# Kernel optimization log

Hardware: AMD Instinct MI355X
Metric: run time of the kernel (lower is better)

Reference implementation:

```python
import jax, jax.numpy as jnp
import numpy as np

HEADS = 16
DIM_HEAD = 64
QUERY_DIM = 1024
CONTEXT_DIM = 1024
INNER = HEADS * DIM_HEAD  # 1024


def setup_inputs() -> dict:
    key = jax.random.key(0)
    k1, k2, k3, k4, k5, k6, k7 = jax.random.split(key, 7)
    b, nq, nk = 2, 2048, 2048
    q = jax.random.normal(k1, (b, nq, QUERY_DIM), dtype=jnp.float32)
    context = jax.random.normal(k2, (b, nk, CONTEXT_DIM), dtype=jnp.float32)
    # True = masked out (filled with -inf); keep sparse so no row is fully masked
    mask = jax.random.randint(k3, (b, nk), 0, 2).astype(bool) & jax.random.randint(k7, (b, nk), 0, 2).astype(bool)
    s = 0.02
    Wq = jax.random.normal(k4, (QUERY_DIM, INNER), dtype=jnp.float32) * s
    Wkv = jax.random.normal(k5, (CONTEXT_DIM, 2 * INNER), dtype=jnp.float32) * s
    Wout = jax.random.normal(k6, (INNER, QUERY_DIM), dtype=jnp.float32) * s
    b_out = jnp.zeros((QUERY_DIM,), dtype=jnp.float32)
    return {"q": q, "context": context, "mask": mask, "Wq": Wq, "Wkv": Wkv, "Wout": Wout, "b_out": b_out}


def reference(q, context, mask, Wq, Wkv, Wout, b_out):
    b, nq, _ = q.shape
    nk = context.shape[1]
    h, dh = HEADS, DIM_HEAD
    scale = dh ** -0.5
    qp = q @ Wq                              # [b, nq, h*dh]
    k, v = jnp.split(context @ Wkv, 2, -1)   # each [b, nk, h*dh]
    qh = qp.reshape(b, nq, h, dh).transpose(0, 2, 1, 3)  # [b, h, nq, dh]
    kh = k.reshape(b, nk, h, dh).transpose(0, 2, 1, 3)
    vh = v.reshape(b, nk, h, dh).transpose(0, 2, 1, 3)
    attn = jnp.einsum('bhid,bhjd->bhij', qh, kh) * scale  # [b, h, nq, nk]
    attn = jnp.where(mask[:, None, None, :], -jnp.inf, attn)
    attn = jax.nn.softmax(attn, axis=-1)
    out = jnp.einsum('bhij,bhjd->bhid', attn, vh)         # [b, h, nq, dh]
    out = out.transpose(0, 2, 1, 3).reshape(b, nq, h * dh)
    return out @ Wout + b_out
```

## Files before the change

kernel.cpp:

```cpp
#include <hip/hip_runtime.h>
#include <stdint.h>

typedef unsigned short u16;
typedef __attribute__((ext_vector_type(8))) short bf16x8;
typedef __attribute__((ext_vector_type(4))) float f32x4;
typedef __attribute__((ext_vector_type(4))) u16 u16x4;

#define DEVI __device__ __forceinline__

DEVI u16 f2bf(float x){
  uint32_t u = __float_as_uint(x);
  u += 0x7fffu + ((u >> 16) & 1u);
  return (u16)(u >> 16);
}

DEVI void gload_lds16(const void* g, void* l){
  __builtin_amdgcn_global_load_lds((__attribute__((address_space(1))) const void*)g,
                                   (__attribute__((address_space(3))) void*)l,
                                   16, 0, 0);
}

__global__ __launch_bounds__(256) void k_prep(const float* __restrict__ q,
                                              const float* __restrict__ ctx,
                                              const int* __restrict__ m,
                                              u16* __restrict__ qb, u16* __restrict__ cb,
                                              float* __restrict__ mf){
  const int b = blockIdx.x;
  if (b < 2048){
    const float* s = (b < 1024) ? q : ctx;
    u16* d = (b < 1024) ? qb : cb;
    const int base = (b & 1023) << 12;
    #pragma unroll
    for (int it = 0; it < 4; ++it){
      const int i = base + (it << 10) + (threadIdx.x << 2);
      const float4 v = *(const float4*)(s + i);
      u16x4 o = { f2bf(v.x), f2bf(v.y), f2bf(v.z), f2bf(v.w) };
      *(u16x4*)(d + i) = o;
    }
  } else {
    for (int i = threadIdx.x; i < 4096; i += 256) mf[i] = m[i] ? -1e30f : 0.0f;
  }
}

__global__ __launch_bounds__(256) void k_tr3(const float* __restrict__ Wq,
                                             const float* __restrict__ Wkv,
                                             const float* __restrict__ Wo,
                                             u16* __restrict__ WqT, u16* __restrict__ WkvT,
                                             u16* __restrict__ WoT){
  const int z = blockIdx.z;
  if (z != 1 && blockIdx.x >= 16) return;
  const float* s = (z == 0) ? Wq : (z == 1) ? Wkv : Wo;
  u16* d = (z == 0) ? WqT : (z == 1) ? WkvT : WoT;
  const int R = 1024, C = (z == 1) ? 2048 : 1024;
  __shared__ float t[64][65];
  const int x = threadIdx.x, y = threadIdx.y;
  const int r0 = blockIdx.y * 64, c0 = blockIdx.x * 64;
  #pragma unroll
  for (int yy = y; yy < 64; yy += 4) t[yy][x] = s[(size_t)(r0 + yy) * C + c0 + x];
  __syncthreads();
  #pragma unroll
  for (int yy = y; yy < 64; yy += 4) d[(size_t)(c0 + yy) * R + r0 + x] = f2bf(t[x][yy]);
}

__global__ __launch_bounds__(256, 2)
void k_gemm01(const u16* __restrict__ Aq, const u16* __restrict__ Ac,
              const u16* __restrict__ Bq, const u16* __restrict__ Bkv,
              u16* __restrict__ QPb, u16* __restrict__ Kbb, u16* __restrict__ Vtb)
{
  __shared__ __align__(16) u16 As[128 * 64];
  __shared__ __align__(16) u16 Bs[128 * 64];
  const int tid = threadIdx.x;
  const int lane = tid & 63, wave = tid >> 6;
  const int g = lane >> 4, l16 = lane & 15;
  const int bx = blockIdx.x;
  const bool isq = bx < 8;
  const u16* A = isq ? Aq : Ac;
  const u16* B = isq ? Bq : Bkv;
  const int brow = blockIdx.y << 7, bcol = (isq ? bx : bx - 8) << 7;
  const int wr = wave >> 1, wc = wave & 1;
  f32x4 acc[4][4] = {};

  for (int kt = 0; kt < 16; ++kt){
    const int k0 = kt << 6;
    #pragma unroll
    for (int i = 0; i < 4; ++i){
      const int c = i * 256 + tid;
      const int row = c >> 3;
      const int sc = ((c & 7) ^ (row & 7)) << 3;
      gload_lds16(A + (size_t)(brow + row) * 1024 + k0 + sc, (char*)As + (i * 4 + wave) * 1024);
      gload_lds16(B + (size_t)(bcol + row) * 1024 + k0 + sc, (char*)Bs + (i * 4 + wave) * 1024);
    }
    __syncthreads();
    #pragma unroll
    for (int kk = 0; kk < 2; ++kk){
      bf16x8 a[4], b[4];
      #pragma unroll
      for (int mi = 0; mi < 4; ++mi){
        const int r = wr * 64 + mi * 16 + l16;
        a[mi] = *(const bf16x8*)((const char*)As + r * 128 + (((kk << 6) + (g << 4)) ^ ((r & 7) << 4)));
      }
      #pragma unroll
      for (int ni = 0; ni < 4; ++ni){
        const int r = wc * 64 + ni * 16 + l16;
        b[ni] = *(const bf16x8*)((const char*)Bs + r * 128 + (((kk << 6) + (g << 4)) ^ ((r & 7) << 4)));
      }
      #pragma unroll
      for (int mi = 0; mi < 4; ++mi)
        #pragma unroll
        for (int ni = 0; ni < 4; ++ni)
          acc[mi][ni] = __builtin_amdgcn_mfma_f32_16x16x32_bf16(a[mi], b[ni], acc[mi][ni], 0, 0, 0);
    }
    __syncthreads();
  }

  #pragma unroll
  for (int mi = 0; mi < 4; ++mi){
    #pragma unroll
    for (int ni = 0; ni < 4; ++ni){
      #pragma unroll
      for (int r = 0; r < 4; ++r){
        const int row = brow + wr * 64 + mi * 16 + g * 4 + r;
        const int col = bcol + wc * 64 + ni * 16 + l16;
        const float v = acc[mi][ni][r];
        const int bb = row >> 11, qi = row & 2047;
        if (isq){
          const int h = col >> 6, dd = col & 63;
          QPb[(size_t)((bb << 4) + h) * 131072 + (qi << 6) + dd] = f2bf(v * 0.125f);
        } else if (col < 1024){
          const int h = col >> 6, dd = col & 63;
          Kbb[(size_t)((bb << 4) + h) * 131072 + (qi << 6) + dd] = f2bf(v);
        } else {
          const int c2 = col - 1024, h = c2 >> 6, dd = c2 & 63;
          Vtb[(size_t)((bb << 4) + h) * 131072 + (dd << 11) + qi] = f2bf(v);
        }
      }
    }
  }
}

__global__ __launch_bounds__(256, 2)
void k_gemm2(const u16* __restrict__ A, const u16* __restrict__ B,
             float* __restrict__ D, const float* __restrict__ bias)
{
  __shared__ __align__(16) u16 As[128 * 64];
  __shared__ __align__(16) u16 Bs[128 * 64];
  const int tid = threadIdx.x;
  const int lane = tid & 63, wave = tid >> 6;
  const int g = lane >> 4, l16 = lane & 15;
  const int brow = blockIdx.y << 7, bcol = blockIdx.x << 7;
  const int wr = wave >> 1, wc = wave & 1;
  f32x4 acc[4][4] = {};

  for (int kt = 0; kt < 16; ++kt){
    const int k0 = kt << 6;
    #pragma unroll
    for (int i = 0; i < 4; ++i){
      const int c = i * 256 + tid;
      const int row = c >> 3;
      const int sc = ((c & 7) ^ (row & 7)) << 3;
      gload_lds16(A + (size_t)(brow + row) * 1024 + k0 + sc, (char*)As + (i * 4 + wave) * 1024);
      gload_lds16(B + (size_t)(bcol + row) * 1024 + k0 + sc, (char*)Bs + (i * 4 + wave) * 1024);
    }
    __syncthreads();
    #pragma unroll
    for (int kk = 0; kk < 2; ++kk){
      bf16x8 a[4], b[4];
      #pragma unroll
      for (int mi = 0; mi < 4; ++mi){
        const int r = wr * 64 + mi * 16 + l16;
        a[mi] = *(const bf16x8*)((const char*)As + r * 128 + (((kk << 6) + (g << 4)) ^ ((r & 7) << 4)));
      }
      #pragma unroll
      for (int ni = 0; ni < 4; ++ni){
        const int r = wc * 64 + ni * 16 + l16;
        b[ni] = *(const bf16x8*)((const char*)Bs + r * 128 + (((kk << 6) + (g << 4)) ^ ((r & 7) << 4)));
      }
      #pragma unroll
      for (int mi = 0; mi < 4; ++mi)
        #pragma unroll
        for (int ni = 0; ni < 4; ++ni)
          acc[mi][ni] = __builtin_amdgcn_mfma_f32_16x16x32_bf16(a[mi], b[ni], acc[mi][ni], 0, 0, 0);
    }
    __syncthreads();
  }

  #pragma unroll
  for (int mi = 0; mi < 4; ++mi)
    #pragma unroll
    for (int ni = 0; ni < 4; ++ni)
      #pragma unroll
      for (int r = 0; r < 4; ++r){
        const int row = brow + wr * 64 + mi * 16 + g * 4 + r;
        const int col = bcol + wc * 64 + ni * 16 + l16;
        D[(size_t)row * 1024 + col] = acc[mi][ni][r] + bias[col];
      }
}

__global__ __launch_bounds__(512, 4)
void k_attn(const u16* __restrict__ QP, const u16* __restrict__ Kb,
            const u16* __restrict__ Vt, const float* __restrict__ mf,
            u16* __restrict__ AO)
{
  __shared__ __align__(16) u16 Ks[2][64 * 64];
  __shared__ __align__(16) u16 Vs[2][64 * 64];
  __shared__ __align__(16) u16 Ps[8 * 16 * 64];
  const int tid = threadIdx.x, lane = tid & 63, wave = tid >> 6;
  const int g = lane >> 4, l16 = lane & 15;
  const int bh = blockIdx.y;
  const int q0 = blockIdx.x << 7;
  const u16* Qg = QP + (size_t)bh * 131072;
  const u16* Kg = Kb + (size_t)bh * 131072;
  const u16* Vg = Vt + (size_t)bh * 131072;
  const float* mrow = mf + (bh >> 4) * 2048;

  const int srow = tid >> 3;
  const int ssc  = ((tid & 7) ^ (srow & 7)) << 3;

  bf16x8 aq[2];
  #pragma unroll
  for (int kk = 0; kk < 2; ++kk)
    aq[kk] = *(const bf16x8*)(Qg + (size_t)(q0 + (wave << 4) + l16) * 64 + (kk << 5) + (g << 3));

  f32x4 o[4] = {};
  float ms[4], ls[4];
  #pragma unroll
  for (int r = 0; r < 4; ++r){ ms[r] = -1e30f; ls[r] = 0.f; }

  gload_lds16(Kg + (size_t)srow * 64 + ssc, (char*)Ks[0] + wave * 1024);
  gload_lds16(Vg + (size_t)srow * 2048 + ssc, (char*)Vs[0] + wave * 1024);

  int cur = 0;
  for (int jt = 0; jt < 32; ++jt){
    const int j0 = jt << 6;
    __syncthreads();
    if (jt < 31){
      gload_lds16(Kg + (size_t)(j0 + 64 + srow) * 64 + ssc, (char*)Ks[cur ^ 1] + wave * 1024);
      gload_lds16(Vg + (size_t)srow * 2048 + j0 + 64 + ssc, (char*)Vs[cur ^ 1] + wave * 1024);
    }
    float madd[4];
    #pragma unroll
    for (int ni = 0; ni < 4; ++ni) madd[ni] = mrow[j0 + ni * 16 + l16];

    f32x4 s[4] = {};
    #pragma unroll
    for (int kk = 0; kk < 2; ++kk){
      bf16x8 bk[4];
      #pragma unroll
      for (int ni = 0; ni < 4; ++ni){
        const int r = ni * 16 + l16;
        bk[ni] = *(const bf16x8*)((const char*)Ks[cur] + r * 128 + (((kk << 6) + (g << 4)) ^ ((r & 7) << 4)));
      }
      #pragma unroll
      for (int ni = 0; ni < 4; ++ni)
        s[ni] = __builtin_amdgcn_mfma_f32_16x16x32_bf16(aq[kk], bk[ni], s[ni], 0, 0, 0);
    }

    #pragma unroll
    for (int ni = 0; ni < 4; ++ni)
      #pragma unroll
      for (int r = 0; r < 4; ++r)
        s[ni][r] += madd[ni];
    #pragma unroll
    for (int r = 0; r < 4; ++r){
      float mx = fmaxf(fmaxf(s[0][r], s[1][r]), fmaxf(s[2][r], s[3][r]));
      #pragma unroll
      for (int d = 1; d < 16; d <<= 1) mx = fmaxf(mx, __shfl_xor(mx, d));
      const float mnew = fmaxf(ms[r], mx);
      const float rf = __expf(ms[r] - mnew);
      ms[r] = mnew;
      float rs = 0.f;
      #pragma unroll
      for (int ni = 0; ni < 4; ++ni){
        const float sv = s[ni][r];
        const float pv = (sv < -1e29f) ? 0.f : __expf(sv - mnew);
        s[ni][r] = pv;
        rs += pv;
      }
      #pragma unroll
      for (int d = 1; d < 16; d <<= 1) rs += __shfl_xor(rs, d);
      ls[r] = ls[r] * rf + rs;
      #pragma unroll
      for (int nd = 0; nd < 4; ++nd) o[nd][r] *= rf;
    }

    #pragma unroll
    for (int ni = 0; ni < 4; ++ni)
      #pragma unroll
      for (int r = 0; r < 4; ++r){
        const int q = (g << 2) + r;
        const int key2 = (ni * 16 + l16) << 1;
        *(u16*)((char*)Ps + (wave << 11) + (q << 7) + (key2 ^ ((q & 7) << 4))) = f2bf(s[ni][r]);
      }

    #pragma unroll
    for (int kk2 = 0; kk2 < 2; ++kk2){
      bf16x8 ap, bv[4];
      ap = *(const bf16x8*)((const char*)Ps + (wave << 11) + (l16 << 7) + (((kk2 << 6) + (g << 4)) ^ ((l16 & 7) << 4)));
      #pragma unroll
      for (int nd = 0; nd < 4; ++nd){
        const int r = nd * 16 + l16;
        bv[nd] = *(const bf16x8*)((const char*)Vs[cur] + r * 128 + (((kk2 << 6) + (g << 4)) ^ ((r & 7) << 4)));
      }
      #pragma unroll
      for (int nd = 0; nd < 4; ++nd)
        o[nd] = __builtin_amdgcn_mfma_f32_16x16x32_bf16(ap, bv[nd], o[nd], 0, 0, 0);
    }
    cur ^= 1;
  }

  const int b = bh >> 4, h = bh & 15;
  #pragma unroll
  for (int nd = 0; nd < 4; ++nd)
    #pragma unroll
    for (int r = 0; r < 4; ++r){
      const int qi = q0 + (wave << 4) + (g << 2) + r;
      const int col = h * 64 + nd * 16 + l16;
      AO[(size_t)(b * 2048 + qi) * 1024 + col] = f2bf(o[nd][r] / ls[r]);
    }
}

extern "C" void kernel_launch(void* const* d_in, const int* in_sizes, int n_in,
                              void* d_out, int out_size, void* d_ws, size_t ws_size,
                              hipStream_t stream)
{
  (void)in_sizes; (void)n_in; (void)out_size; (void)ws_size;
  const float* q   = (const float*)d_in[0];
  const float* ctx = (const float*)d_in[1];
  const int*   msk = (const int*)d_in[2];
  const float* Wq  = (const float*)d_in[3];
  const float* Wkv = (const float*)d_in[4];
  const float* Wo  = (const float*)d_in[5];
  const float* bo  = (const float*)d_in[6];
  float* out = (float*)d_out;

  char* ws = (char*)d_ws;
  u16*   q_bf = (u16*)(ws);
  u16*   c_bf = (u16*)(ws + (size_t)( 8u << 20));
  u16*   WqT  = (u16*)(ws + (size_t)(16u << 20));
  u16*   WkvT = (u16*)(ws + (size_t)(18u << 20));
  u16*   WoT  = (u16*)(ws + (size_t)(22u << 20));
  float* mf   = (float*)(ws + (size_t)(24u << 20));
  u16*   QPb  = (u16*)(ws + (size_t)(25u << 20));
  u16*   Kbb  = (u16*)(ws + (size_t)(33u << 20));
  u16*   Vtb  = (u16*)(ws + (size_t)(41u << 20));
  u16*   AOb  = (u16*)(ws + (size_t)(49u << 20));

  k_prep  <<<dim3(2049),      dim3(256),   0, stream>>>(q, ctx, msk, q_bf, c_bf, mf);
  k_tr3   <<<dim3(32, 16, 3), dim3(64, 4), 0, stream>>>(Wq, Wkv, Wo, WqT, WkvT, WoT);
  k_gemm01<<<dim3(24, 32),    dim3(256),   0, stream>>>(q_bf, c_bf, WqT, WkvT, QPb, Kbb, Vtb);
  k_attn  <<<dim3(16, 32),    dim3(512),   0, stream>>>(QPb, Kbb, Vtb, mf, AOb);
  k_gemm2 <<<dim3(8, 32),     dim3(256),   0, stream>>>(AOb, WoT, out, bo);
}
```

Before: 272.9 us.

## Rewrite attention with 32x32 MFMA, register-resident P, bitmask, lazy rescale

The attention kernel is restructured so each of 4 waves owns 32 query rows and computes S transposed (K·Q) with 32x32x16 MFMAs. The P tile is repacked in registers via v_permlane32_swap instead of going through LDS. The mask is packed into bits and the scale is folded into Q with log2(e) so exp2 can be used. The running-max rescale is skipped unless the max grows by more than 8. This is meant to remove LDS round-trips, mask float loads and redundant exp work, at the cost of higher per-thread register pressure and fewer threads per block.

```diff
diff --git a/kernel.cpp b/kernel.cpp
--- a/kernel.cpp
+++ b/kernel.cpp
@@ -1,9 +1,11 @@
 #include <hip/hip_runtime.h>
 #include <stdint.h>
+#include <math.h>
 
 typedef unsigned short u16;
 typedef __attribute__((ext_vector_type(8))) short bf16x8;
 typedef __attribute__((ext_vector_type(4))) float f32x4;
+typedef __attribute__((ext_vector_type(16))) float f32x16;
 typedef __attribute__((ext_vector_type(4))) u16 u16x4;
 
 #define DEVI __device__ __forceinline__
@@ -14,17 +16,25 @@
   return (u16)(u >> 16);
 }
 
+DEVI uint32_t pkbf(float lo, float hi){
+  return (uint32_t)f2bf(lo) | ((uint32_t)f2bf(hi) << 16);
+}
+
 DEVI void gload_lds16(const void* g, void* l){
   __builtin_amdgcn_global_load_lds((__attribute__((address_space(1))) const void*)g,
                                    (__attribute__((address_space(3))) void*)l,
                                    16, 0, 0);
 }
 
+DEVI void pl32swap_u(uint32_t& a, uint32_t& b){
+  asm volatile("v_permlane32_swap_b32 %0, %1" : "+&v"(a), "+v"(b));
+}
+
 __global__ __launch_bounds__(256) void k_prep(const float* __restrict__ q,
                                               const float* __restrict__ ctx,
                                               const int* __restrict__ m,
                                               u16* __restrict__ qb, u16* __restrict__ cb,
-                                              float* __restrict__ mf){
+                                              uint32_t* __restrict__ mb){
   const int b = blockIdx.x;
   if (b < 2048){
     const float* s = (b < 1024) ? q : ctx;
@@ -38,7 +48,12 @@
       *(u16x4*)(d + i) = o;
     }
   } else {
-    for (int i = threadIdx.x; i < 4096; i += 256) mf[i] = m[i] ? -1e30f : 0.0f;
+    for (int w = threadIdx.x; w < 128; w += 256){
+      const int bb = w >> 6, wi = w & 63;
+      uint32_t bits = 0;
+      for (int i = 0; i < 32; ++i) bits |= (m[(bb << 11) + (wi << 5) + i] ? 1u : 0u) << i;
+      mb[w] = bits;
+    }
   }
 }
 
@@ -125,7 +140,7 @@
         const int bb = row >> 11, qi = row & 2047;
         if (isq){
           const int h = col >> 6, dd = col & 63;
-          QPb[(size_t)((bb << 4) + h) * 131072 + (qi << 6) + dd] = f2bf(v * 0.125f);
+          QPb[(size_t)((bb << 4) + h) * 131072 + (qi << 6) + dd] = f2bf(v * 0.18033688f);
         } else if (col < 1024){
           const int h = col >> 6, dd = col & 63;
           Kbb[(size_t)((bb << 4) + h) * 131072 + (qi << 6) + dd] = f2bf(v);
@@ -196,127 +211,147 @@
       }
 }
 
-__global__ __launch_bounds__(512, 4)
+__global__ __launch_bounds__(256, 2)
 void k_attn(const u16* __restrict__ QP, const u16* __restrict__ Kb,
-            const u16* __restrict__ Vt, const float* __restrict__ mf,
+            const u16* __restrict__ Vt, const uint32_t* __restrict__ mbits,
             u16* __restrict__ AO)
 {
   __shared__ __align__(16) u16 Ks[2][64 * 64];
   __shared__ __align__(16) u16 Vs[2][64 * 64];
-  __shared__ __align__(16) u16 Ps[8 * 16 * 64];
   const int tid = threadIdx.x, lane = tid & 63, wave = tid >> 6;
-  const int g = lane >> 4, l16 = lane & 15;
+  const int l31 = lane & 31, hi = lane >> 5;
   const int bh = blockIdx.y;
-  const int q0 = blockIdx.x << 7;
+  const int q0 = (blockIdx.x << 7) + (wave << 5);
   const u16* Qg = QP + (size_t)bh * 131072;
   const u16* Kg = Kb + (size_t)bh * 131072;
   const u16* Vg = Vt + (size_t)bh * 131072;
-  const float* mrow = mf + (bh >> 4) * 2048;
-
-  const int srow = tid >> 3;
-  const int ssc  = ((tid & 7) ^ (srow & 7)) << 3;
-
-  bf16x8 aq[2];
-  #pragma unroll
-  for (int kk = 0; kk < 2; ++kk)
-    aq[kk] = *(const bf16x8*)(Qg + (size_t)(q0 + (wave << 4) + l16) * 64 + (kk << 5) + (g << 3));
-
-  f32x4 o[4] = {};
-  float ms[4], ls[4];
-  #pragma unroll
-  for (int r = 0; r < 4; ++r){ ms[r] = -1e30f; ls[r] = 0.f; }
-
-  gload_lds16(Kg + (size_t)srow * 64 + ssc, (char*)Ks[0] + wave * 1024);
-  gload_lds16(Vg + (size_t)srow * 2048 + ssc, (char*)Vs[0] + wave * 1024);
+  const uint32_t* mrow = mbits + (bh >> 4) * 64;
+  const int bpa = hi << 4;
+
+  bf16x8 qf[4];
+  #pragma unroll
+  for (int ks = 0; ks < 4; ++ks)
+    qf[ks] = *(const bf16x8*)(Qg + (size_t)(q0 + l31) * 64 + ks * 16 + hi * 8);
+
+  f32x16 o0 = {}, o1 = {};
+  float ms = -1e30f, ls = 0.f;
+
+  #pragma unroll
+  for (int i = 0; i < 2; ++i){
+    const int row = i * 32 + (tid >> 3);
+    const int sc = ((tid & 7) ^ (row & 7)) << 3;
+    gload_lds16(Kg + (size_t)row * 64 + sc, (char*)Ks[0] + (i * 4 + wave) * 1024);
+    gload_lds16(Vg + (size_t)row * 2048 + sc, (char*)Vs[0] + (i * 4 + wave) * 1024);
+  }
 
   int cur = 0;
   for (int jt = 0; jt < 32; ++jt){
     const int j0 = jt << 6;
     __syncthreads();
     if (jt < 31){
-      gload_lds16(Kg + (size_t)(j0 + 64 + srow) * 64 + ssc, (char*)Ks[cur ^ 1] + wave * 1024);
-      gload_lds16(Vg + (size_t)srow * 2048 + j0 + 64 + ssc, (char*)Vs[cur ^ 1] + wave * 1024);
-    }
-    float madd[4];
-    #pragma unroll
-    for (int ni = 0; ni < 4; ++ni) madd[ni] = mrow[j0 + ni * 16 + l16];
-
-    f32x4 s[4] = {};
-    #pragma unroll
-    for (int kk = 0; kk < 2; ++kk){
-      bf16x8 bk[4];
-      #pragma unroll
-      for (int ni = 0; ni < 4; ++ni){
-        const int r = ni * 16 + l16;
-        bk[ni] = *(const bf16x8*)((const char*)Ks[cur] + r * 128 + (((kk << 6) + (g << 4)) ^ ((r & 7) << 4)));
-      }
-      #pragma unroll
-      for (int ni = 0; ni < 4; ++ni)
-        s[ni] = __builtin_amdgcn_mfma_f32_16x16x32_bf16(aq[kk], bk[ni], s[ni], 0, 0, 0);
-    }
-
-    #pragma unroll
-    for (int ni = 0; ni < 4; ++ni)
-      #pragma unroll
-      for (int r = 0; r < 4; ++r)
-        s[ni][r] += madd[ni];
-    #pragma unroll
-    for (int r = 0; r < 4; ++r){
-      float mx = fmaxf(fmaxf(s[0][r], s[1][r]), fmaxf(s[2][r], s[3][r]));
-      #pragma unroll
-      for (int d = 1; d < 16; d <<= 1) mx = fmaxf(mx, __shfl_xor(mx, d));
-      const float mnew = fmaxf(ms[r], mx);
-      const float rf = __expf(ms[r] - mnew);
-      ms[r] = mnew;
-      float rs = 0.f;
-      #pragma unroll
-      for (int ni = 0; ni < 4; ++ni){
-        const float sv = s[ni][r];
-        const float pv = (sv < -1e29f) ? 0.f : __expf(sv - mnew);
-        s[ni][r] = pv;
-        rs += pv;
-      }
-      #pragma unroll
-      for (int d = 1; d < 16; d <<= 1) rs += __shfl_xor(rs, d);
-      ls[r] = ls[r] * rf + rs;
-      #pragma unroll
-      for (int nd = 0; nd < 4; ++nd) o[nd][r] *= rf;
-    }
-
-    #pragma unroll
-    for (int ni = 0; ni < 4; ++ni)
-      #pragma unroll
-      for (int r = 0; r < 4; ++r){
-        const int q = (g << 2) + r;
-        const int key2 = (ni * 16 + l16) << 1;
-        *(u16*)((char*)Ps + (wave << 11) + (q << 7) + (key2 ^ ((q & 7) << 4))) = f2bf(s[ni][r]);
-      }
-
-    #pragma unroll
-    for (int kk2 = 0; kk2 < 2; ++kk2){
-      bf16x8 ap, bv[4];
-      ap = *(const bf16x8*)((const char*)Ps + (wave << 11) + (l16 << 7) + (((kk2 << 6) + (g << 4)) ^ ((l16 & 7) << 4)));
-      #pragma unroll
-      for (int nd = 0; nd < 4; ++nd){
-        const int r = nd * 16 + l16;
-        bv[nd] = *(const bf16x8*)((const char*)Vs[cur] + r * 128 + (((kk2 << 6) + (g << 4)) ^ ((r & 7) << 4)));
-      }
-      #pragma unroll
-      for (int nd = 0; nd < 4; ++nd)
-        o[nd] = __builtin_amdgcn_mfma_f32_16x16x32_bf16(ap, bv[nd], o[nd], 0, 0, 0);
+      #pragma unroll
+      for (int i = 0; i < 2; ++i){
+        const int row = i * 32 + (tid >> 3);
+        const int sc = ((tid & 7) ^ (row & 7)) << 3;
+        gload_lds16(Kg + (size_t)(j0 + 64 + row) * 64 + sc, (char*)Ks[cur ^ 1] + (i * 4 + wave) * 1024);
+        gload_lds16(Vg + (size_t)row * 2048 + j0 + 64 + sc, (char*)Vs[cur ^ 1] + (i * 4 + wave) * 1024);
+      }
+    }
+
+    f32x16 s0 = {}, s1 = {};
+    #pragma unroll
+    for (int ks = 0; ks < 4; ++ks){
+      const int co = ks * 32 + hi * 16;
+      {
+        const int r = l31;
+        bf16x8 kf = *(const bf16x8*)((const char*)Ks[cur] + r * 128 + (co ^ ((r & 7) << 4)));
+        s0 = __builtin_amdgcn_mfma_f32_32x32x16_bf16(kf, qf[ks], s0, 0, 0, 0);
+      }
+      {
+        const int r = 32 + l31;
+        bf16x8 kf = *(const bf16x8*)((const char*)Ks[cur] + r * 128 + (co ^ ((r & 7) << 4)));
+        s1 = __builtin_amdgcn_mfma_f32_32x32x16_bf16(kf, qf[ks], s1, 0, 0, 0);
+      }
+    }
+
+    const uint32_t mw0 = mrow[(jt << 1) + 0] >> (hi << 2);
+    const uint32_t mw1 = mrow[(jt << 1) + 1] >> (hi << 2);
+    #pragma unroll
+    for (int r = 0; r < 16; ++r){
+      const int c = (r & 3) + ((r >> 2) << 3);
+      s0[r] = fmaf((float)((mw0 >> c) & 1u), -3e38f, s0[r]);
+      s1[r] = fmaf((float)((mw1 >> c) & 1u), -3e38f, s1[r]);
+    }
+
+    float pm = fmaxf(s0[0], s1[0]);
+    #pragma unroll
+    for (int r = 1; r < 16; ++r) pm = fmaxf(pm, fmaxf(s0[r], s1[r]));
+    pm = fmaxf(pm, __shfl_xor(pm, 32));
+
+    if (!__all(pm - ms <= 8.0f)){
+      const float mnew = fmaxf(ms, pm);
+      const float rf = exp2f(ms - mnew);
+      ms = mnew; ls *= rf;
+      #pragma unroll
+      for (int r = 0; r < 16; ++r){
+        const int c = (r & 3) + ((r >> 2) << 3);
+        const float rfr = __int_as_float(__builtin_amdgcn_ds_bpermute(bpa + (c << 2), __float_as_int(rf)));
+        o0[r] *= rfr; o1[r] *= rfr;
+      }
+    }
+
+    float rs = 0.f;
+    #pragma unroll
+    for (int r = 0; r < 16; ++r){
+      s0[r] = exp2f(s0[r] - ms);
+      s1[r] = exp2f(s1[r] - ms);
+      rs += s0[r] + s1[r];
+    }
+    rs += __shfl_xor(rs, 32);
+    ls += rs;
+
+    uint32_t w[4][4];
+    #pragma unroll
+    for (int t = 0; t < 2; ++t){
+      { uint32_t A = pkbf(s0[2*t], s0[2*t+1]),      B = pkbf(s0[4+2*t],  s0[5+2*t]);
+        pl32swap_u(A, B); w[0][t] = A; w[0][2+t] = B; }
+      { uint32_t A = pkbf(s0[8+2*t], s0[9+2*t]),    B = pkbf(s0[12+2*t], s0[13+2*t]);
+        pl32swap_u(A, B); w[1][t] = A; w[1][2+t] = B; }
+      { uint32_t A = pkbf(s1[2*t], s1[2*t+1]),      B = pkbf(s1[4+2*t],  s1[5+2*t]);
+        pl32swap_u(A, B); w[2][t] = A; w[2][2+t] = B; }
+      { uint32_t A = pkbf(s1[8+2*t], s1[9+2*t]),    B = pkbf(s1[12+2*t], s1[13+2*t]);
+        pl32swap_u(A, B); w[3][t] = A; w[3][2+t] = B; }
+    }
+
+    #pragma unroll
+    for (int ks = 0; ks < 4; ++ks){
+      union { uint32_t u[4]; bf16x8 v; } pa;
+      pa.u[0] = w[ks][0]; pa.u[1] = w[ks][1]; pa.u[2] = w[ks][2]; pa.u[3] = w[ks][3];
+      const int co = ks * 32 + hi * 16;
+      {
+        const int r = l31;
+        bf16x8 vf = *(const bf16x8*)((const char*)Vs[cur] + r * 128 + (co ^ ((r & 7) << 4)));
+        o0 = __builtin_amdgcn_mfma_f32_32x32x16_bf16(pa.v, vf, o0, 0, 0, 0);
+      }
+      {
+        const int r = 32 + l31;
+        bf16x8 vf = *(const bf16x8*)((const char*)Vs[cur] + r * 128 + (co ^ ((r & 7) << 4)));
+        o1 = __builtin_amdgcn_mfma_f32_32x32x16_bf16(pa.v, vf, o1, 0, 0, 0);
+      }
     }
     cur ^= 1;
   }
 
+  const float linv = 1.0f / ls;
   const int b = bh >> 4, h = bh & 15;
   #pragma unroll
-  for (int nd = 0; nd < 4; ++nd)
-    #pragma unroll
-    for (int r = 0; r < 4; ++r){
-      const int qi = q0 + (wave << 4) + (g << 2) + r;
-      const int col = h * 64 + nd * 16 + l16;
-      AO[(size_t)(b * 2048 + qi) * 1024 + col] = f2bf(o[nd][r] / ls[r]);
-    }
+  for (int r = 0; r < 16; ++r){
+    const int c = (r & 3) + ((r >> 2) << 3);
+    const float lr = __int_as_float(__builtin_amdgcn_ds_bpermute(bpa + (c << 2), __float_as_int(linv)));
+    const int qi = q0 + c + (hi << 2);
+    AO[(size_t)(b * 2048 + qi) * 1024 + h * 64 + l31]      = f2bf(o0[r] * lr);
+    AO[(size_t)(b * 2048 + qi) * 1024 + h * 64 + 32 + l31] = f2bf(o1[r] * lr);
+  }
 }
 
 extern "C" void kernel_launch(void* const* d_in, const int* in_sizes, int n_in,
@@ -334,20 +369,20 @@
   float* out = (float*)d_out;
 
   char* ws = (char*)d_ws;
-  u16*   q_bf = (u16*)(ws);
-  u16*   c_bf = (u16*)(ws + (size_t)( 8u << 20));
-  u16*   WqT  = (u16*)(ws + (size_t)(16u << 20));
-  u16*   WkvT = (u16*)(ws + (size_t)(18u << 20));
-  u16*   WoT  = (u16*)(ws + (size_t)(22u << 20));
-  float* mf   = (float*)(ws + (size_t)(24u << 20));
-  u16*   QPb  = (u16*)(ws + (size_t)(25u << 20));
-  u16*   Kbb  = (u16*)(ws + (size_t)(33u << 20));
-  u16*   Vtb  = (u16*)(ws + (size_t)(41u << 20));
-  u16*   AOb  = (u16*)(ws + (size_t)(49u << 20));
-
-  k_prep  <<<dim3(2049),      dim3(256),   0, stream>>>(q, ctx, msk, q_bf, c_bf, mf);
+  u16*      q_bf  = (u16*)(ws);
+  u16*      c_bf  = (u16*)(ws + (size_t)( 8u << 20));
+  u16*      WqT   = (u16*)(ws + (size_t)(16u << 20));
+  u16*      WkvT  = (u16*)(ws + (size_t)(18u << 20));
+  u16*      WoT   = (u16*)(ws + (size_t)(22u << 20));
+  uint32_t* mbits = (uint32_t*)(ws + (size_t)(24u << 20));
+  u16*      QPb   = (u16*)(ws + (size_t)(25u << 20));
+  u16*      Kbb   = (u16*)(ws + (size_t)(33u << 20));
+  u16*      Vtb   = (u16*)(ws + (size_t)(41u << 20));
+  u16*      AOb   = (u16*)(ws + (size_t)(49u << 20));
+
+  k_prep  <<<dim3(2049),      dim3(256),   0, stream>>>(q, ctx, msk, q_bf, c_bf, mbits);
   k_tr3   <<<dim3(32, 16, 3), dim3(64, 4), 0, stream>>>(Wq, Wkv, Wo, WqT, WkvT, WoT);
   k_gemm01<<<dim3(24, 32),    dim3(256),   0, stream>>>(q_bf, c_bf, WqT, WkvT, QPb, Kbb, Vtb);
-  k_attn  <<<dim3(16, 32),    dim3(512),   0, stream>>>(QPb, Kbb, Vtb, mf, AOb);
+  k_attn  <<<dim3(16, 32),    dim3(256),   0, stream>>>(QPb, Kbb, Vtb, mbits, AOb);
   k_gemm2 <<<dim3(8, 32),     dim3(256),   0, stream>>>(AOb, WoT, out, bo);
 }
```

After: 251.8 us. 1.08x faster.
